# Performance work log

Hardware: AMD Instinct MI355X
Metric: run time of the kernel (lower is better)

Reference implementation:

```python
import jax, jax.numpy as jnp
import numpy as np

ATTN = 512
HIDDEN = 1024
NUM_GENES = 2048
NUM_GF = 4


def setup_inputs() -> dict:
    key = jax.random.key(0)
    ks = jax.random.split(key, 8)
    s = 0.1
    return {
        "genes": jax.random.normal(ks[0], (32, NUM_GENES, NUM_GF), dtype=jnp.float32),
        "smiles": jax.random.normal(ks[1], (32, 2048, HIDDEN), dtype=jnp.float32),
        "w_num_gene_features": s * jax.random.normal(ks[2], (NUM_GF,), dtype=jnp.float32),
        "w_genes": s * jax.random.normal(ks[3], (NUM_GENES, ATTN), dtype=jnp.float32),
        "b_genes": s * jax.random.normal(ks[4], (ATTN,), dtype=jnp.float32),
        "w_smiles": s * jax.random.normal(ks[5], (HIDDEN, ATTN), dtype=jnp.float32),
        "b_smiles": s * jax.random.normal(ks[6], (ATTN,), dtype=jnp.float32),
        "v": s * jax.random.normal(ks[7], (ATTN,), dtype=jnp.float32),
    }


def reference(genes, smiles, w_num_gene_features, w_genes, b_genes, w_smiles, b_smiles, v):
    # genes: [B, G, F] -> collapse feature axis: [B, G]
    genes_collapsed = jnp.einsum("bgf,f->bg", genes, w_num_gene_features)
    # gene context projection: [B, A]
    x = jnp.einsum("bg,ga->ba", genes_collapsed, w_genes) + b_genes
    # smiles projection: [B, T, A]
    y = jnp.einsum("bth,ha->bta", smiles, w_smiles) + b_smiles
    h = jnp.tanh(x[:, None, :] + y)  # [B, T, A]
    scores = jnp.einsum("bta,a->bt", h, v)  # [B, T]
    alphas = jax.nn.softmax(scores, axis=-1)  # [B, T]
    # attention-weighted sum over sequence: [B, H]
    return jnp.einsum("bth,bt->bh", smiles, alphas)
```

## Files before the change

kernel.cpp:

```cpp
#include <hip/hip_runtime.h>


typedef __bf16 bf16_t;
typedef bf16_t bf16x8 __attribute__((ext_vector_type(8)));
typedef float f32x4 __attribute__((ext_vector_type(4)));

__device__ __forceinline__ unsigned short f32_to_bf16_rne(float f) {
    unsigned int u = __builtin_bit_cast(unsigned int, f);
    u = (u + 0x7FFFu + ((u >> 16) & 1u)) >> 16;
    return (unsigned short)u;
}

__device__ __forceinline__ float fast_tanh(float x) {
    float cx = fminf(fmaxf(x, -30.f), 30.f);
    float e = __expf(2.f * cx);
    return (e - 1.f) / (e + 1.f);
}

__global__ void k0b_pack(const float* __restrict__ w, unsigned short* __restrict__ Bp) {
    int bid  = blockIdx.x;
    int lane = threadIdx.x;
    int atile = bid >> 5, gks = bid & 31;
    int col = atile * 16 + (lane & 15);
    int k0  = gks * 32 + (lane >> 4) * 8;
    unsigned short us[8];
#pragma unroll
    for (int e = 0; e < 8; ++e)
        us[e] = f32_to_bf16_rne(w[(size_t)(k0 + e) * 512 + col]);
    *(uint4*)(Bp + (size_t)bid * 512 + lane * 8) = *(const uint4*)us;
}

__global__ void k1a_gc(const float4* __restrict__ genes, const float* __restrict__ wngf,
                       float* __restrict__ gc) {
    int i = blockIdx.x * 256 + threadIdx.x;
    float4 g = genes[i];
    gc[i] = g.x * wngf[0] + g.y * wngf[1] + g.z * wngf[2] + g.w * wngf[3];
}

__global__ void k1b_x(const float* __restrict__ gc, const float* __restrict__ wg,
                      float* __restrict__ x) {
    __shared__ float gcl[256];
    int bx = blockIdx.x;
    int b = bx >> 4, ah = (bx >> 3) & 1, gch = bx & 7;
    int g0 = gch * 256;
    gcl[threadIdx.x] = gc[b * 2048 + g0 + threadIdx.x];
    __syncthreads();
    int a = ah * 256 + threadIdx.x;
    float s = 0.f;
#pragma unroll 8
    for (int g = 0; g < 256; ++g) s += gcl[g] * wg[(size_t)(g0 + g) * 512 + a];
    atomicAdd(&x[b * 512 + a], s);
}

__global__ __launch_bounds__(512, 4) void k2_scores(
    const float* __restrict__ smiles,
    const unsigned short* __restrict__ Bp,
    const float* __restrict__ xraw,
    const float* __restrict__ b_genes,
    const float* __restrict__ b_smiles,
    const float* __restrict__ v,
    float* __restrict__ scores)
{
    __shared__ unsigned short A_lds[2 * 64 * 128];
    const int tid  = threadIdx.x;
    const int wave = tid >> 6;
    const int lane = tid & 63;
    const int l15  = lane & 15;
    const int l4   = lane >> 4;
    const int gm0  = blockIdx.x * 64;
    const int bidx = gm0 >> 11;
    const int wbase = wave * 64;

    const unsigned short* bpp = Bp + (size_t)(wave * 128) * 512 + lane * 8;

    const int srow = tid >> 3;
    const int scol = (tid & 7) * 16;
    const float* sptr = smiles + (size_t)(gm0 + srow) * 1024 + scol;
    const int sswz = (srow & 7) << 4;
    char* wr0 = (char*)A_lds + srow * 256 + (((tid & 7) * 32) ^ sswz);
    char* wr1 = (char*)A_lds + srow * 256 + ((((tid & 7) * 32) + 16) ^ sswz);

    float4 st0, st1, st2, st3;

    const f32x4 zero4 = {0.f, 0.f, 0.f, 0.f};
    f32x4 acc[4][4];
#pragma unroll
    for (int mt = 0; mt < 4; ++mt)
#pragma unroll
        for (int nt = 0; nt < 4; ++nt)
            acc[mt][nt] = zero4;

#define LOADREGS(kt)                                   \
    {   const float* p = sptr + (kt) * 128;            \
        st0 = *(const float4*)(p);                     \
        st1 = *(const float4*)(p + 4);                 \
        st2 = *(const float4*)(p + 8);                 \
        st3 = *(const float4*)(p + 12); }

#define CONVWRITE(buf)                                                     \
    {   union { unsigned short us[8]; uint4 u4; } pa, pb;                  \
        pa.us[0] = f32_to_bf16_rne(st0.x); pa.us[1] = f32_to_bf16_rne(st0.y); \
        pa.us[2] = f32_to_bf16_rne(st0.z); pa.us[3] = f32_to_bf16_rne(st0.w); \
        pa.us[4] = f32_to_bf16_rne(st1.x); pa.us[5] = f32_to_bf16_rne(st1.y); \
        pa.us[6] = f32_to_bf16_rne(st1.z); pa.us[7] = f32_to_bf16_rne(st1.w); \
        pb.us[0] = f32_to_bf16_rne(st2.x); pb.us[1] = f32_to_bf16_rne(st2.y); \
        pb.us[2] = f32_to_bf16_rne(st2.z); pb.us[3] = f32_to_bf16_rne(st2.w); \
        pb.us[4] = f32_to_bf16_rne(st3.x); pb.us[5] = f32_to_bf16_rne(st3.y); \
        pb.us[6] = f32_to_bf16_rne(st3.z); pb.us[7] = f32_to_bf16_rne(st3.w); \
        *(uint4*)(wr0 + (buf) * 16384) = pa.u4;                            \
        *(uint4*)(wr1 + (buf) * 16384) = pb.u4; }

#define COMPUTE(cur, kt)                                                      \
    _Pragma("unroll")                                                         \
    for (int ks4 = 0; ks4 < 4; ++ks4) {                                       \
        int gks = (kt) * 4 + ks4;                                             \
        bf16x8 af[4], bfb[4];                                                 \
        _Pragma("unroll")                                                     \
        for (int nt = 0; nt < 4; ++nt)                                        \
            bfb[nt] = *(const bf16x8*)(bpp + (nt * 32 + gks) * 512);          \
        _Pragma("unroll")                                                     \
        for (int mt = 0; mt < 4; ++mt) {                                      \
            int row = mt * 16 + l15;                                          \
            int byteoff = (cur) * 16384 + row * 256 +                         \
                          ((ks4 * 64 + l4 * 16) ^ ((row & 7) << 4));          \
            af[mt] = *(const bf16x8*)((const char*)A_lds + byteoff);          \
        }                                                                     \
        __builtin_amdgcn_s_setprio(1);                                        \
        _Pragma("unroll")                                                     \
        for (int mt = 0; mt < 4; ++mt)                                        \
            _Pragma("unroll")                                                 \
            for (int nt = 0; nt < 4; ++nt)                                    \
                acc[mt][nt] = __builtin_amdgcn_mfma_f32_16x16x32_bf16(        \
                    af[mt], bfb[nt], acc[mt][nt], 0, 0, 0);                   \
        __builtin_amdgcn_s_setprio(0);                                        \
    }

    LOADREGS(0);
    CONVWRITE(0);
    __syncthreads();

    int cur = 0;
#pragma unroll 1
    for (int kt = 0; kt < 7; ++kt) {
        LOADREGS(kt + 1);
        COMPUTE(cur, kt);
        CONVWRITE(cur ^ 1);
        __syncthreads();
        cur ^= 1;
    }
    COMPUTE(cur, 7);

#undef LOADREGS
#undef CONVWRITE
#undef COMPUTE

    float xbv[4], vv[4];
#pragma unroll
    for (int nt = 0; nt < 4; ++nt) {
        int a = wbase + nt * 16 + l15;
        xbv[nt] = xraw[bidx * 512 + a] + b_genes[a] + b_smiles[a];
        vv[nt]  = v[a];
    }
    float rs[4][4];
#pragma unroll
    for (int mt = 0; mt < 4; ++mt)
#pragma unroll
        for (int r = 0; r < 4; ++r)
            rs[mt][r] = 0.f;
#pragma unroll
    for (int mt = 0; mt < 4; ++mt)
#pragma unroll
        for (int nt = 0; nt < 4; ++nt)
#pragma unroll
            for (int r = 0; r < 4; ++r)
                rs[mt][r] += vv[nt] * fast_tanh(acc[mt][nt][r] + xbv[nt]);
#pragma unroll
    for (int mt = 0; mt < 4; ++mt)
#pragma unroll
        for (int r = 0; r < 4; ++r) {
            float s = rs[mt][r];
            s += __shfl_xor(s, 1);
            s += __shfl_xor(s, 2);
            s += __shfl_xor(s, 4);
            s += __shfl_xor(s, 8);
            rs[mt][r] = s;
        }
    if (l15 == 0) {
#pragma unroll
        for (int mt = 0; mt < 4; ++mt)
#pragma unroll
            for (int r = 0; r < 4; ++r)
                atomicAdd(&scores[gm0 + mt * 16 + l4 * 4 + r], rs[mt][r]);
    }
}

__global__ void k3_softmax(const float* __restrict__ scores, float* __restrict__ alphas) {
    __shared__ float redmax[4], redsum[4];
    int b = blockIdx.x, tid = threadIdx.x;
    int wave = tid >> 6;
    float sv[8];
    float mx = -1e30f;
#pragma unroll
    for (int i = 0; i < 8; ++i) {
        sv[i] = scores[b * 2048 + i * 256 + tid];
        mx = fmaxf(mx, sv[i]);
    }
#pragma unroll
    for (int m = 32; m >= 1; m >>= 1) mx = fmaxf(mx, __shfl_xor(mx, m));
    if ((tid & 63) == 0) redmax[wave] = mx;
    __syncthreads();
    mx = fmaxf(fmaxf(redmax[0], redmax[1]), fmaxf(redmax[2], redmax[3]));
    float sum = 0.f;
#pragma unroll
    for (int i = 0; i < 8; ++i) {
        sv[i] = __expf(sv[i] - mx);
        sum += sv[i];
    }
#pragma unroll
    for (int m = 32; m >= 1; m >>= 1) sum += __shfl_xor(sum, m);
    if ((tid & 63) == 0) redsum[wave] = sum;
    __syncthreads();
    sum = redsum[0] + redsum[1] + redsum[2] + redsum[3];
    float inv = 1.f / sum;
#pragma unroll
    for (int i = 0; i < 8; ++i) alphas[b * 2048 + i * 256 + tid] = sv[i] * inv;
}

__global__ void k4_out(const float* __restrict__ smiles,
                       const float* __restrict__ alphas,
                       float* __restrict__ out)
{
    int bx = blockIdx.x;
    int b  = bx >> 4;
    int tc = bx & 15;
    int h  = threadIdx.x * 4;
    const float* sb = smiles + ((size_t)b * 2048 + tc * 128) * 1024;
    const float* al = alphas + b * 2048 + tc * 128;
    float4 acc = {0.f, 0.f, 0.f, 0.f};
#pragma unroll 4
    for (int t = 0; t < 128; ++t) {
        float a = al[t];
        float4 sv = *(const float4*)(sb + (size_t)t * 1024 + h);
        acc.x += a * sv.x;
        acc.y += a * sv.y;
        acc.z += a * sv.z;
        acc.w += a * sv.w;
    }
    float* o = out + b * 1024 + h;
    atomicAdd(o + 0, acc.x);
    atomicAdd(o + 1, acc.y);
    atomicAdd(o + 2, acc.z);
    atomicAdd(o + 3, acc.w);
}

extern "C" void kernel_launch(void* const* d_in, const int* in_sizes, int n_in,
                              void* d_out, int out_size, void* d_ws, size_t ws_size,
                              hipStream_t stream) {
    const float* genes    = (const float*)d_in[0];
    const float* smiles   = (const float*)d_in[1];
    const float* w_ngf    = (const float*)d_in[2];
    const float* w_genes  = (const float*)d_in[3];
    const float* b_genes  = (const float*)d_in[4];
    const float* w_smiles = (const float*)d_in[5];
    const float* b_smiles = (const float*)d_in[6];
    const float* v        = (const float*)d_in[7];
    float* out = (float*)d_out;

    char* ws = (char*)d_ws;
    unsigned short* Bp = (unsigned short*)(ws);
    float* gc     = (float*)(ws + (1 << 20));
    float* x      = (float*)(ws + (1 << 20) + (256 << 10));
    float* scores = (float*)(ws + (1 << 20) + (320 << 10));
    float* alphas = (float*)(ws + (1 << 20) + (576 << 10));

    hipMemsetAsync(out, 0, (size_t)32 * 1024 * sizeof(float), stream);
    hipMemsetAsync(x, 0, (size_t)(64 + 256) * 1024, stream);

    k0b_pack<<<1024, 64, 0, stream>>>(w_smiles, Bp);
    k1a_gc<<<256, 256, 0, stream>>>((const float4*)genes, w_ngf, gc);
    k1b_x<<<512, 256, 0, stream>>>(gc, w_genes, x);
    k2_scores<<<1024, 512, 0, stream>>>(smiles, Bp, x, b_genes, b_smiles, v, scores);
    k3_softmax<<<32, 256, 0, stream>>>(scores, alphas);
    k4_out<<<512, 256, 0, stream>>>(smiles, alphas, out);
}
```

Baseline: 162.5 us.

## Switch score GEMM to 32x32x16 MFMA tiles and split output reduction finer

The scores GEMM moves from 16x16x32 to 32x32x16 bf16 MFMA instructions, with a 2x2 tile per wave. The weight packing layout, the LDS swizzle and the epilogue row mapping are rebuilt to match. This cuts the fragment loads per MFMA and raises arithmetic intensity per LDS read. Separately, the weighted-sum kernel splits the sequence into 64-row chunks across twice as many blocks for more parallelism, which doubles the number of atomic adds.

```diff
diff --git a/kernel.cpp b/kernel.cpp
--- a/kernel.cpp
+++ b/kernel.cpp
@@ -3,7 +3,7 @@
 
 typedef __bf16 bf16_t;
 typedef bf16_t bf16x8 __attribute__((ext_vector_type(8)));
-typedef float f32x4 __attribute__((ext_vector_type(4)));
+typedef float f32x16 __attribute__((ext_vector_type(16)));
 
 __device__ __forceinline__ unsigned short f32_to_bf16_rne(float f) {
     unsigned int u = __builtin_bit_cast(unsigned int, f);
@@ -20,9 +20,9 @@
 __global__ void k0b_pack(const float* __restrict__ w, unsigned short* __restrict__ Bp) {
     int bid  = blockIdx.x;
     int lane = threadIdx.x;
-    int atile = bid >> 5, gks = bid & 31;
-    int col = atile * 16 + (lane & 15);
-    int k0  = gks * 32 + (lane >> 4) * 8;
+    int atile2 = bid >> 6, gks16 = bid & 63;
+    int col = atile2 * 32 + (lane & 31);
+    int k0  = gks16 * 16 + (lane >> 5) * 8;
     unsigned short us[8];
 #pragma unroll
     for (int e = 0; e < 8; ++e)
@@ -61,34 +61,34 @@
     const float* __restrict__ v,
     float* __restrict__ scores)
 {
-    __shared__ unsigned short A_lds[2 * 64 * 128];
+    __shared__ char A_lds[2 * 64 * 256];
     const int tid  = threadIdx.x;
     const int wave = tid >> 6;
     const int lane = tid & 63;
-    const int l15  = lane & 15;
-    const int l4   = lane >> 4;
+    const int l31  = lane & 31;
+    const int hi   = lane >> 5;
     const int gm0  = blockIdx.x * 64;
     const int bidx = gm0 >> 11;
     const int wbase = wave * 64;
 
-    const unsigned short* bpp = Bp + (size_t)(wave * 128) * 512 + lane * 8;
+    const unsigned short* bpp = Bp + (size_t)(wave * 2) * 64 * 512 + lane * 8;
 
     const int srow = tid >> 3;
-    const int scol = (tid & 7) * 16;
-    const float* sptr = smiles + (size_t)(gm0 + srow) * 1024 + scol;
-    const int sswz = (srow & 7) << 4;
+    const float* sptr = smiles + (size_t)(gm0 + srow) * 1024 + (tid & 7) * 16;
+    const int sswz = (srow & 15) << 4;
     char* wr0 = (char*)A_lds + srow * 256 + (((tid & 7) * 32) ^ sswz);
     char* wr1 = (char*)A_lds + srow * 256 + ((((tid & 7) * 32) + 16) ^ sswz);
 
     float4 st0, st1, st2, st3;
 
-    const f32x4 zero4 = {0.f, 0.f, 0.f, 0.f};
-    f32x4 acc[4][4];
-#pragma unroll
-    for (int mt = 0; mt < 4; ++mt)
-#pragma unroll
-        for (int nt = 0; nt < 4; ++nt)
-            acc[mt][nt] = zero4;
+    f32x16 acc[2][2];
+#pragma unroll
+    for (int mt = 0; mt < 2; ++mt)
+#pragma unroll
+        for (int nt = 0; nt < 2; ++nt)
+#pragma unroll
+            for (int r = 0; r < 16; ++r)
+                acc[mt][nt][r] = 0.f;
 
 #define LOADREGS(kt)                                   \
     {   const float* p = sptr + (kt) * 128;            \
@@ -110,29 +110,28 @@
         *(uint4*)(wr0 + (buf) * 16384) = pa.u4;                            \
         *(uint4*)(wr1 + (buf) * 16384) = pb.u4; }
 
-#define COMPUTE(cur, kt)                                                      \
-    _Pragma("unroll")                                                         \
-    for (int ks4 = 0; ks4 < 4; ++ks4) {                                       \
-        int gks = (kt) * 4 + ks4;                                             \
-        bf16x8 af[4], bfb[4];                                                 \
-        _Pragma("unroll")                                                     \
-        for (int nt = 0; nt < 4; ++nt)                                        \
-            bfb[nt] = *(const bf16x8*)(bpp + (nt * 32 + gks) * 512);          \
-        _Pragma("unroll")                                                     \
-        for (int mt = 0; mt < 4; ++mt) {                                      \
-            int row = mt * 16 + l15;                                          \
-            int byteoff = (cur) * 16384 + row * 256 +                         \
-                          ((ks4 * 64 + l4 * 16) ^ ((row & 7) << 4));          \
-            af[mt] = *(const bf16x8*)((const char*)A_lds + byteoff);          \
-        }                                                                     \
-        __builtin_amdgcn_s_setprio(1);                                        \
-        _Pragma("unroll")                                                     \
-        for (int mt = 0; mt < 4; ++mt)                                        \
-            _Pragma("unroll")                                                 \
-            for (int nt = 0; nt < 4; ++nt)                                    \
-                acc[mt][nt] = __builtin_amdgcn_mfma_f32_16x16x32_bf16(        \
-                    af[mt], bfb[nt], acc[mt][nt], 0, 0, 0);                   \
-        __builtin_amdgcn_s_setprio(0);                                        \
+#define COMPUTE(cur, kt)                                                        \
+    _Pragma("unroll")                                                           \
+    for (int ks = 0; ks < 8; ++ks) {                                            \
+        bf16x8 af[2], bfb[2];                                                   \
+        _Pragma("unroll")                                                       \
+        for (int nt = 0; nt < 2; ++nt)                                          \
+            bfb[nt] = *(const bf16x8*)(bpp + (size_t)(nt * 64 + (kt) * 8 + ks) * 512); \
+        _Pragma("unroll")                                                       \
+        for (int mt = 0; mt < 2; ++mt) {                                        \
+            int row = mt * 32 + l31;                                            \
+            int byteoff = (cur) * 16384 + row * 256 +                           \
+                          ((ks * 32 + hi * 16) ^ ((row & 15) << 4));            \
+            af[mt] = *(const bf16x8*)(A_lds + byteoff);                         \
+        }                                                                       \
+        __builtin_amdgcn_s_setprio(1);                                          \
+        _Pragma("unroll")                                                       \
+        for (int mt = 0; mt < 2; ++mt)                                          \
+            _Pragma("unroll")                                                   \
+            for (int nt = 0; nt < 2; ++nt)                                      \
+                acc[mt][nt] = __builtin_amdgcn_mfma_f32_32x32x16_bf16(          \
+                    af[mt], bfb[nt], acc[mt][nt], 0, 0, 0);                     \
+        __builtin_amdgcn_s_setprio(0);                                          \
     }
 
     LOADREGS(0);
@@ -154,43 +153,40 @@
 #undef CONVWRITE
 #undef COMPUTE
 
-    float xbv[4], vv[4];
-#pragma unroll
-    for (int nt = 0; nt < 4; ++nt) {
-        int a = wbase + nt * 16 + l15;
+    float xbv[2], vv[2];
+#pragma unroll
+    for (int nt = 0; nt < 2; ++nt) {
+        int a = wbase + nt * 32 + l31;
         xbv[nt] = xraw[bidx * 512 + a] + b_genes[a] + b_smiles[a];
         vv[nt]  = v[a];
     }
-    float rs[4][4];
-#pragma unroll
-    for (int mt = 0; mt < 4; ++mt)
-#pragma unroll
-        for (int r = 0; r < 4; ++r)
-            rs[mt][r] = 0.f;
-#pragma unroll
-    for (int mt = 0; mt < 4; ++mt)
-#pragma unroll
-        for (int nt = 0; nt < 4; ++nt)
-#pragma unroll
-            for (int r = 0; r < 4; ++r)
-                rs[mt][r] += vv[nt] * fast_tanh(acc[mt][nt][r] + xbv[nt]);
-#pragma unroll
-    for (int mt = 0; mt < 4; ++mt)
-#pragma unroll
-        for (int r = 0; r < 4; ++r) {
-            float s = rs[mt][r];
+#pragma unroll
+    for (int mt = 0; mt < 2; ++mt) {
+        float rs[16];
+#pragma unroll
+        for (int r = 0; r < 16; ++r) rs[r] = 0.f;
+#pragma unroll
+        for (int nt = 0; nt < 2; ++nt)
+#pragma unroll
+            for (int r = 0; r < 16; ++r)
+                rs[r] += vv[nt] * fast_tanh(acc[mt][nt][r] + xbv[nt]);
+#pragma unroll
+        for (int r = 0; r < 16; ++r) {
+            float s = rs[r];
             s += __shfl_xor(s, 1);
             s += __shfl_xor(s, 2);
             s += __shfl_xor(s, 4);
             s += __shfl_xor(s, 8);
-            rs[mt][r] = s;
+            s += __shfl_xor(s, 16);
+            rs[r] = s;
         }
-    if (l15 == 0) {
-#pragma unroll
-        for (int mt = 0; mt < 4; ++mt)
-#pragma unroll
-            for (int r = 0; r < 4; ++r)
-                atomicAdd(&scores[gm0 + mt * 16 + l4 * 4 + r], rs[mt][r]);
+        if (l31 == 0) {
+#pragma unroll
+            for (int r = 0; r < 16; ++r) {
+                int row = (r & 3) + 8 * (r >> 2) + 4 * hi;
+                atomicAdd(&scores[gm0 + mt * 32 + row], rs[r]);
+            }
+        }
     }
 }
 
@@ -231,14 +227,14 @@
                        float* __restrict__ out)
 {
     int bx = blockIdx.x;
-    int b  = bx >> 4;
-    int tc = bx & 15;
+    int b  = bx >> 5;
+    int tc = bx & 31;
     int h  = threadIdx.x * 4;
-    const float* sb = smiles + ((size_t)b * 2048 + tc * 128) * 1024;
-    const float* al = alphas + b * 2048 + tc * 128;
+    const float* sb = smiles + ((size_t)b * 2048 + tc * 64) * 1024;
+    const float* al = alphas + b * 2048 + tc * 64;
     float4 acc = {0.f, 0.f, 0.f, 0.f};
 #pragma unroll 4
-    for (int t = 0; t < 128; ++t) {
+    for (int t = 0; t < 64; ++t) {
         float a = al[t];
         float4 sv = *(const float4*)(sb + (size_t)t * 1024 + h);
         acc.x += a * sv.x;
@@ -281,5 +277,5 @@
     k1b_x<<<512, 256, 0, stream>>>(gc, w_genes, x);
     k2_scores<<<1024, 512, 0, stream>>>(smiles, Bp, x, b_genes, b_smiles, v, scores);
     k3_softmax<<<32, 256, 0, stream>>>(scores, alphas);
-    k4_out<<<512, 256, 0, stream>>>(smiles, alphas, out);
-}
+    k4_out<<<1024, 256, 0, stream>>>(smiles, alphas, out);
+}
```

Measured after the change: 182.9 us. 12.6% more time.
